# Kernel optimization log

Hardware: AMD Instinct MI355X
Metric: run time of the kernel (lower is better)

## Reference

```python
import jax, jax.numpy as jnp
import numpy as np

N = 128000   # total nodes (64 instances x 2000 nodes)
G = 64       # num graphs / instances
H = 128      # hidden_dim
IN = 3       # in_dim
L = 4        # embedding_l
E = 1024000
EPC = 512000
EMC = 512000
BN_EPS = 1e-5


def seg_mean(vals, idx, n):
    s = jax.ops.segment_sum(vals, idx, num_segments=n)
    c = jax.ops.segment_sum(jnp.ones((idx.shape[0], 1), vals.dtype), idx, num_segments=n)
    return s / jnp.maximum(c, 1.0)


def gin_layer(x, src, dst, W1, b1, g, beta, W2, b2):
    # GINConv(aggr='mean', eps=0): MLP(x + mean_{j->i} x_j), MLP = Lin-BN-ReLU-Lin
    agg = seg_mean(x[src], dst, N)
    z = (x + agg) @ W1 + b1
    mu = jnp.mean(z, axis=0)
    var = jnp.var(z, axis=0)
    z = (z - mu) / jnp.sqrt(var + BN_EPS) * g + beta   # BatchNorm1d (batch stats)
    z = jax.nn.relu(z)
    return z @ W2 + b2


def gat_conv(x, src, dst, W, asrc, adst, b):
    # PyG GATConv, heads=1: h=Wx; alpha=softmax_dst(leaky_relu(a_s.h_src + a_d.h_dst))
    h = x @ W                                           # [N, H]
    logits = jax.nn.leaky_relu((h * asrc).sum(-1)[src] + (h * adst).sum(-1)[dst], 0.2)
    m = jax.ops.segment_max(logits, dst, num_segments=N)
    a = jnp.exp(logits - m[dst])
    s = jax.ops.segment_sum(a, dst, num_segments=N)
    coef = a / (s[dst] + 1e-16)                         # self loops guarantee s > 0
    out = jax.ops.segment_sum(h[src] * coef[:, None], dst, num_segments=N)
    return out + b


def add_self_loops(ei):
    loops = jnp.arange(N, dtype=ei.dtype)
    return jnp.concatenate([ei[0], loops]), jnp.concatenate([ei[1], loops])


def setup_inputs() -> dict:
    key = jax.random.key(0)
    ks = iter(jax.random.split(key, 40))
    d = {}
    d['x'] = jax.random.normal(next(ks), (N, IN), dtype=jnp.float32)
    d['edge_index'] = jax.random.randint(next(ks), (2, E), 0, N)
    d['edge_index_pc'] = jax.random.randint(next(ks), (2, EPC), 0, N)
    d['edge_index_mc'] = jax.random.randint(next(ks), (2, EMC), 0, N)
    d['batch'] = jnp.repeat(jnp.arange(G), N // G)
    d['num_instances'] = G
    sc_in = 1.0 / np.sqrt(IN)
    sc_h = 1.0 / np.sqrt(H)
    # GIN layer 0 (in_dim=3) and layers 1..3 stacked
    d['gin0_W1'] = jax.random.normal(next(ks), (IN, H), jnp.float32) * sc_in
    d['gin0_b1'] = jnp.zeros((H,), jnp.float32)
    d['gin0_g'] = jnp.ones((H,), jnp.float32)
    d['gin0_beta'] = jnp.zeros((H,), jnp.float32)
    d['gin0_W2'] = jax.random.normal(next(ks), (H, H), jnp.float32) * sc_h
    d['gin0_b2'] = jnp.zeros((H,), jnp.float32)
    d['ginr_W1'] = jax.random.normal(next(ks), (L - 1, H, H), jnp.float32) * sc_h
    d['ginr_b1'] = jnp.zeros((L - 1, H), jnp.float32)
    d['ginr_g'] = jnp.ones((L - 1, H), jnp.float32)
    d['ginr_beta'] = jnp.zeros((L - 1, H), jnp.float32)
    d['ginr_W2'] = jax.random.normal(next(ks), (L - 1, H, H), jnp.float32) * sc_h
    d['ginr_b2'] = jnp.zeros((L - 1, H), jnp.float32)
    # DGHAN GAT params: layer 0 (in_dim=3), layers 1..3 (in=H); 2 convs (pc, mc) each
    d['gat0_W'] = jax.random.normal(next(ks), (2, IN, H), jnp.float32) * sc_in
    d['gat0_asrc'] = jax.random.normal(next(ks), (2, H), jnp.float32) * sc_h
    d['gat0_adst'] = jax.random.normal(next(ks), (2, H), jnp.float32) * sc_h
    d['gat0_bias'] = jnp.zeros((2, H), jnp.float32)
    d['gatr_W'] = jax.random.normal(next(ks), (L - 1, 2, H, H), jnp.float32) * sc_h
    d['gatr_asrc'] = jax.random.normal(next(ks), (L - 1, 2, H), jnp.float32) * sc_h
    d['gatr_adst'] = jax.random.normal(next(ks), (L - 1, 2, H), jnp.float32) * sc_h
    d['gatr_bias'] = jnp.zeros((L - 1, 2, H), jnp.float32)
    return d


def reference(x, edge_index, edge_index_pc, edge_index_mc, batch,
              gin0_W1, gin0_b1, gin0_g, gin0_beta, gin0_W2, gin0_b2,
              ginr_W1, ginr_b1, ginr_g, ginr_beta, ginr_W2, ginr_b2,
              gat0_W, gat0_asrc, gat0_adst, gat0_bias,
              gatr_W, gatr_asrc, gatr_adst, gatr_bias,
              num_instances):
    src, dst = edge_index[0], edge_index[1]
    # ---- GIN branch ----
    h = gin_layer(x, src, dst, gin0_W1, gin0_b1, gin0_g, gin0_beta, gin0_W2, gin0_b2)
    node_pool = h
    g_pool = seg_mean(h, batch, num_instances)
    for l in range(L - 1):
        h = gin_layer(h, src, dst, ginr_W1[l], ginr_b1[l], ginr_g[l], ginr_beta[l],
                      ginr_W2[l], ginr_b2[l])
        node_pool = node_pool + h
        g_pool = g_pool + seg_mean(h, batch, num_instances)
    # ---- DGHAN branch ----
    pc_src, pc_dst = add_self_loops(edge_index_pc)
    mc_src, mc_dst = add_self_loops(edge_index_mc)

    def dghan_layer(hn, W, asrc, adst, b):
        h_pc = jax.nn.elu(gat_conv(hn, pc_src, pc_dst, W[0], asrc[0], adst[0], b[0]))
        h_mc = jax.nn.elu(gat_conv(hn, mc_src, mc_dst, W[1], asrc[1], adst[1], b[1]))
        return 0.5 * (h_pc + h_mc)

    hd = dghan_layer(x, gat0_W, gat0_asrc, gat0_adst, gat0_bias)
    for l in range(L - 1):
        hd = dghan_layer(hd, gatr_W[l], gatr_asrc[l], gatr_adst[l], gatr_bias[l])
    graph_dghan = jnp.mean(hd.reshape(num_instances, -1, H), axis=1)
    # ---- fuse ----
    node_embed = jnp.concatenate([node_pool, hd], axis=-1)     # [N, 2H]
    graph_embed = jnp.concatenate([g_pool, graph_dghan], axis=-1)  # [G, 2H]
    return node_embed, graph_embed
```

## Files before the change

### kernel.cpp

```cpp
#include <hip/hip_runtime.h>
#include <cstdint>

#define NN 128000
#define GG 64
#define HH 128
#define EG 1024000
#define EPCV 512000
#define NPG 2000

static __device__ __forceinline__ float lrelu(float x){ return x > 0.f ? x : 0.2f*x; }
static __device__ __forceinline__ float f4get(const float4& v, int j){
  return j==0 ? v.x : j==1 ? v.y : j==2 ? v.z : v.w;
}

__global__ void k_seti(int* p, int n, int v){
  int i = blockIdx.x*blockDim.x + threadIdx.x;
  if(i < n) p[i] = v;
}
__global__ void k_setf(float* p, int n){
  int i = blockIdx.x*blockDim.x + threadIdx.x;
  if(i < n) p[i] = 0.f;
}

__global__ void k_hist(const int* __restrict__ dst, int E, int* __restrict__ counts){
  int i = blockIdx.x*blockDim.x + threadIdx.x;
  if(i < E) atomicAdd(&counts[dst[i]], 1);
}
__global__ void k_scan1(const int* __restrict__ counts, int* __restrict__ rowptr, int* __restrict__ bsums){
  __shared__ int lds[256];
  int t = threadIdx.x, b = blockIdx.x;
  int i0 = b*512 + t*2;
  int s0 = counts[i0], s1 = counts[i0+1];
  int pair = s0 + s1;
  lds[t] = pair; __syncthreads();
  for(int off=1; off<256; off<<=1){
    int v = (t >= off) ? lds[t-off] : 0;
    __syncthreads();
    lds[t] += v;
    __syncthreads();
  }
  int excl = lds[t] - pair;
  rowptr[i0+1] = excl + s0;
  rowptr[i0+2] = excl + pair;
  if(t == 255) bsums[b] = lds[t];
}
__global__ void k_scan2(int* bsums, int nb){
  __shared__ int lds[256];
  int t = threadIdx.x;
  int v = (t < nb) ? bsums[t] : 0;
  lds[t] = v; __syncthreads();
  for(int off=1; off<256; off<<=1){
    int u = (t >= off) ? lds[t-off] : 0;
    __syncthreads();
    lds[t] += u;
    __syncthreads();
  }
  if(t < nb) bsums[t] = lds[t] - v;
}
__global__ void k_scan3(int* __restrict__ rowptr, const int* __restrict__ bsums){
  int i = blockIdx.x*blockDim.x + threadIdx.x;
  if(i >= NN) return;
  rowptr[i+1] += bsums[i >> 9];
  if(i == 0) rowptr[0] = 0;
}
__global__ void k_fill(const int* __restrict__ rowptr, int* __restrict__ fill){
  int i = blockIdx.x*blockDim.x + threadIdx.x;
  if(i < NN) fill[i] = rowptr[i];
}
__global__ void k_scatter(const int* __restrict__ src, const int* __restrict__ dst, int E,
                          int* __restrict__ fill, int* __restrict__ colarr){
  int i = blockIdx.x*blockDim.x + threadIdx.x;
  if(i >= E) return;
  int pos = atomicAdd(&fill[dst[i]], 1);
  colarr[pos] = src[i];
}
__global__ void k_scatter_loops(int* __restrict__ fill, int* __restrict__ colarr){
  int i = blockIdx.x*blockDim.x + threadIdx.x;
  if(i >= NN) return;
  int pos = atomicAdd(&fill[i], 1);
  colarr[pos] = i;
}

__global__ __launch_bounds__(256) void k_segmean3(const float* __restrict__ x, const int* __restrict__ rp,
                           const int* __restrict__ col, float* __restrict__ y,
                           float* __restrict__ part){
  __shared__ float sp[4][9];
  int i = blockIdx.x*256 + threadIdx.x;
  int b = rp[i], e = rp[i+1];
  float a0=0.f, a1=0.f, a2=0.f;
  for(int j=b; j<e; ++j){
    int s = col[j];
    a0 += x[s*3]; a1 += x[s*3+1]; a2 += x[s*3+2];
  }
  float inv = 1.f / fmaxf((float)(e-b), 1.f);
  float y0 = x[i*3]   + a0*inv;
  float y1 = x[i*3+1] + a1*inv;
  float y2 = x[i*3+2] + a2*inv;
  y[i*3] = y0; y[i*3+1] = y1; y[i*3+2] = y2;
  float p[9] = {y0,y1,y2, y0*y0,y0*y1,y0*y2, y1*y1,y1*y2, y2*y2};
  #pragma unroll
  for(int off=1; off<64; off<<=1)
    #pragma unroll
    for(int j=0;j<9;++j) p[j] += __shfl_xor(p[j], off, 64);
  int lane = threadIdx.x & 63, wv = threadIdx.x >> 6;
  if(lane == 0)
    #pragma unroll
    for(int j=0;j<9;++j) sp[wv][j] = p[j];
  __syncthreads();
  int t = threadIdx.x;
  if(t < 9) part[blockIdx.x*9 + t] = sp[0][t] + sp[1][t] + sp[2][t] + sp[3][t];
}


__global__ __launch_bounds__(256) void k_segmean128(const float* __restrict__ h, const int* __restrict__ rp,
                             const int* __restrict__ col, float* __restrict__ y){
  int gid = blockIdx.x*256 + threadIdx.x;
  int w = gid >> 4, c0 = (gid & 15)*8;
  int b = rp[w], e = rp[w+1];
  float s0x=0.f,s0y=0.f,s0z=0.f,s0w=0.f, s1x=0.f,s1y=0.f,s1z=0.f,s1w=0.f;
  int j = b;
  for(; j+2 <= e; j += 2){
    int n0 = col[j], n1 = col[j+1];
    const float* p0 = h + (size_t)n0*HH + c0;
    const float* p1 = h + (size_t)n1*HH + c0;
    float4 u0 = *(const float4*)p0, u1 = *(const float4*)(p0+4);
    float4 v0 = *(const float4*)p1, v1 = *(const float4*)(p1+4);
    s0x += u0.x + v0.x; s0y += u0.y + v0.y; s0z += u0.z + v0.z; s0w += u0.w + v0.w;
    s1x += u1.x + v1.x; s1y += u1.y + v1.y; s1z += u1.z + v1.z; s1w += u1.w + v1.w;
  }
  if(j < e){
    const float* p0 = h + (size_t)col[j]*HH + c0;
    float4 u0 = *(const float4*)p0, u1 = *(const float4*)(p0+4);
    s0x += u0.x; s0y += u0.y; s0z += u0.z; s0w += u0.w;
    s1x += u1.x; s1y += u1.y; s1z += u1.z; s1w += u1.w;
  }
  float inv = 1.f / fmaxf((float)(e-b), 1.f);
  const float* sp = h + (size_t)w*HH + c0;
  float4 e0 = *(const float4*)sp, e1 = *(const float4*)(sp+4);
  float4 o0, o1;
  o0.x = e0.x + s0x*inv; o0.y = e0.y + s0y*inv; o0.z = e0.z + s0z*inv; o0.w = e0.w + s0w*inv;
  o1.x = e1.x + s1x*inv; o1.y = e1.y + s1y*inv; o1.z = e1.z + s1z*inv; o1.w = e1.w + s1w*inv;
  *(float4*)(y + (size_t)w*HH + c0)     = o0;
  *(float4*)(y + (size_t)w*HH + c0 + 4) = o1;
}

__global__ __launch_bounds__(256) void k_gat_agg(const float* __restrict__ hW, const int* __restrict__ rp,
                          const int* __restrict__ col, const float* __restrict__ sd,
                          const float* __restrict__ ddv, float* __restrict__ out,
                          const float* __restrict__ P, const float* __restrict__ bpc,
                          const float* __restrict__ bmc, float* __restrict__ out2){
  int gid = blockIdx.x*256 + threadIdx.x;
  int w = gid >> 4, c0 = (gid & 15)*8;
  int b = rp[w], e = rp[w+1];
  float dv = ddv[w];
  float s = 0.f;
  float a0x=0.f,a0y=0.f,a0z=0.f,a0w=0.f, a1x=0.f,a1y=0.f,a1z=0.f,a1w=0.f;
  int j = b;
  for(; j+2 <= e; j += 2){
    int n0 = col[j], n1 = col[j+1];
    float wt0 = expf(fminf(lrelu(sd[n0] + dv), 80.f));
    float wt1 = expf(fminf(lrelu(sd[n1] + dv), 80.f));
    const float* p0 = hW + (size_t)n0*HH + c0;
    const float* p1 = hW + (size_t)n1*HH + c0;
    float4 u0 = *(const float4*)p0, u1 = *(const float4*)(p0+4);
    float4 v0 = *(const float4*)p1, v1 = *(const float4*)(p1+4);
    s += wt0 + wt1;
    a0x += wt0*u0.x + wt1*v0.x; a0y += wt0*u0.y + wt1*v0.y;
    a0z += wt0*u0.z + wt1*v0.z; a0w += wt0*u0.w + wt1*v0.w;
    a1x += wt0*u1.x + wt1*v1.x; a1y += wt0*u1.y + wt1*v1.y;
    a1z += wt0*u1.z + wt1*v1.z; a1w += wt0*u1.w + wt1*v1.w;
  }
  if(j < e){
    int n0 = col[j];
    float wt0 = expf(fminf(lrelu(sd[n0] + dv), 80.f));
    const float* p0 = hW + (size_t)n0*HH + c0;
    float4 u0 = *(const float4*)p0, u1 = *(const float4*)(p0+4);
    s += wt0;
    a0x += wt0*u0.x; a0y += wt0*u0.y; a0z += wt0*u0.z; a0w += wt0*u0.w;
    a1x += wt0*u1.x; a1y += wt0*u1.y; a1z += wt0*u1.z; a1w += wt0*u1.w;
  }
  float inv = 1.f / (s + 1e-16f);
  a0x*=inv; a0y*=inv; a0z*=inv; a0w*=inv;
  a1x*=inv; a1y*=inv; a1z*=inv; a1w*=inv;
  if(P){
    const float* pp = P + (size_t)w*HH + c0;
    float4 p0 = *(const float4*)pp, p1 = *(const float4*)(pp+4);
    float4 bp0 = *(const float4*)(bpc + c0), bp1 = *(const float4*)(bpc + c0 + 4);
    float4 bm0 = *(const float4*)(bmc + c0), bm1 = *(const float4*)(bmc + c0 + 4);
    float q0 = p0.x + bp0.x; q0 = q0 > 0.f ? q0 : expm1f(q0);
    float q1 = p0.y + bp0.y; q1 = q1 > 0.f ? q1 : expm1f(q1);
    float q2 = p0.z + bp0.z; q2 = q2 > 0.f ? q2 : expm1f(q2);
    float q3 = p0.w + bp0.w; q3 = q3 > 0.f ? q3 : expm1f(q3);
    float q4 = p1.x + bp1.x; q4 = q4 > 0.f ? q4 : expm1f(q4);
    float q5 = p1.y + bp1.y; q5 = q5 > 0.f ? q5 : expm1f(q5);
    float q6 = p1.z + bp1.z; q6 = q6 > 0.f ? q6 : expm1f(q6);
    float q7 = p1.w + bp1.w; q7 = q7 > 0.f ? q7 : expm1f(q7);
    float r0 = a0x + bm0.x; r0 = r0 > 0.f ? r0 : expm1f(r0);
    float r1 = a0y + bm0.y; r1 = r1 > 0.f ? r1 : expm1f(r1);
    float r2 = a0z + bm0.z; r2 = r2 > 0.f ? r2 : expm1f(r2);
    float r3 = a0w + bm0.w; r3 = r3 > 0.f ? r3 : expm1f(r3);
    float r4 = a1x + bm1.x; r4 = r4 > 0.f ? r4 : expm1f(r4);
    float r5 = a1y + bm1.y; r5 = r5 > 0.f ? r5 : expm1f(r5);
    float r6 = a1z + bm1.z; r6 = r6 > 0.f ? r6 : expm1f(r6);
    float r7 = a1w + bm1.w; r7 = r7 > 0.f ? r7 : expm1f(r7);
    float4 o0 = make_float4(0.5f*(q0+r0), 0.5f*(q1+r1), 0.5f*(q2+r2), 0.5f*(q3+r3));
    float4 o1 = make_float4(0.5f*(q4+r4), 0.5f*(q5+r5), 0.5f*(q6+r6), 0.5f*(q7+r7));
    *(float4*)(out + (size_t)w*HH + c0)     = o0;
    *(float4*)(out + (size_t)w*HH + c0 + 4) = o1;
    if(out2){
      *(float4*)&out2[(size_t)w*256 + 128 + c0]     = o0;
      *(float4*)&out2[(size_t)w*256 + 128 + c0 + 4] = o1;
    }
  } else {
    *(float4*)(out + (size_t)w*HH + c0)     = make_float4(a0x, a0y, a0z, a0w);
    *(float4*)(out + (size_t)w*HH + c0 + 4) = make_float4(a1x, a1y, a1z, a1w);
  }
}

__global__ __launch_bounds__(256) void k_mm3(const float* __restrict__ A,
        const float* __restrict__ W,
        const float* __restrict__ asrc, const float* __restrict__ adst,
        float* __restrict__ sd, float* __restrict__ dd, float* __restrict__ out){
  int t = threadIdx.x;
  int r = blockIdx.x*8 + (t >> 5);
  int lane = t & 31, c0 = lane*4;
  float a0 = A[r*3], a1 = A[r*3+1], a2 = A[r*3+2];
  float v[4];
  #pragma unroll
  for(int j=0; j<4; ++j){
    int c = c0 + j;
    v[j] = a0*W[c] + a1*W[128+c] + a2*W[256+c];
  }
  *(float4*)&out[(size_t)r*128 + c0] = make_float4(v[0],v[1],v[2],v[3]);
  float s = 0.f, d = 0.f;
  #pragma unroll
  for(int j=0; j<4; ++j){ s += v[j]*asrc[c0+j]; d += v[j]*adst[c0+j]; }
  #pragma unroll
  for(int off=1; off<32; off<<=1){ s += __shfl_xor(s, off, 64); d += __shfl_xor(d, off, 64); }
  if(lane == 0){ sd[r] = s; dd[r] = d; }
}


#define MM_COMPUTE_CH(BUFIDX, K0) { \
  _Pragma("unroll") \
  for(int j_=0; j_<8; ++j_){ \
    float4 a0 = *(float4*)&sA[BUFIDX][j_][rg8]; \
    float4 a1 = *(float4*)&sA[BUFIDX][j_][rg8+4]; \
    float4 w0 = *(float4*)&sW[(K0)+j_][c0a]; \
    float4 w1 = *(float4*)&sW[(K0)+j_][c0b]; \
    float ar[8] = {a0.x,a0.y,a0.z,a0.w,a1.x,a1.y,a1.z,a1.w}; \
    _Pragma("unroll") \
    for(int rr_=0; rr_<8; ++rr_){ \
      acc[rr_][0] = fmaf(ar[rr_], w0.x, acc[rr_][0]); \
      acc[rr_][1] = fmaf(ar[rr_], w0.y, acc[rr_][1]); \
      acc[rr_][2] = fmaf(ar[rr_], w0.z, acc[rr_][2]); \
      acc[rr_][3] = fmaf(ar[rr_], w0.w, acc[rr_][3]); \
      acc[rr_][4] = fmaf(ar[rr_], w1.x, acc[rr_][4]); \
      acc[rr_][5] = fmaf(ar[rr_], w1.y, acc[rr_][5]); \
      acc[rr_][6] = fmaf(ar[rr_], w1.z, acc[rr_][6]); \
      acc[rr_][7] = fmaf(ar[rr_], w1.w, acc[rr_][7]); \
    } \
  } }

#define MM_STAGE(BUFIDX, CH, SRC) { \
  float4 sv_ = SRC; \
  if(HASBN){ \
    float4 ba_ = *(float4*)&sBNa[(CH)*8 + lk]; \
    float4 bs_ = *(float4*)&sBNsh[(CH)*8 + lk]; \
    sv_.x = fmaxf(fmaf(sv_.x, ba_.x, bs_.x), 0.f); \
    sv_.y = fmaxf(fmaf(sv_.y, ba_.y, bs_.y), 0.f); \
    sv_.z = fmaxf(fmaf(sv_.z, ba_.z, bs_.z), 0.f); \
    sv_.w = fmaxf(fmaf(sv_.w, ba_.w, bs_.w), 0.f); \
  } \
  sA[BUFIDX][lk  ][lrow] = sv_.x; \
  sA[BUFIDX][lk+1][lrow] = sv_.y; \
  sA[BUFIDX][lk+2][lrow] = sv_.z; \
  sA[BUFIDX][lk+3][lrow] = sv_.w; \
  }

template<bool HASBN>
__global__ __launch_bounds__(256) void k_mm128_t(
    const float* __restrict__ A,
    const float* __restrict__ bn_a, const float* __restrict__ bn_sh,
    const float* __restrict__ W, const float* __restrict__ bias,
    float* __restrict__ out, float* __restrict__ pool, int pool_mode,
    const float* __restrict__ asrc, const float* __restrict__ adst,
    float* __restrict__ sd, float* __restrict__ dd,
    float* __restrict__ musum, float* __restrict__ sqsum){
  __shared__ float sW[128][128];
  __shared__ float sA[2][8][128];
  __shared__ float sBNa[128], sBNsh[128];
  __shared__ float ls[128], lq[128];
  int t = threadIdx.x;
  #pragma unroll
  for(int i=0;i<16;++i){
    int f = i*1024 + t*4;
    *(float4*)&sW[f>>7][f&127] = *(const float4*)&W[f];
  }
  if(HASBN && t < 128){ sBNa[t] = bn_a[t]; sBNsh[t] = bn_sh[t]; }
  if(musum && t < 128){ ls[t] = 0.f; lq[t] = 0.f; }
  int row0 = blockIdx.x*128;
  int rg = t >> 4, cg = t & 15;
  int rg8 = rg*8;
  int c0a = cg*4, c0b = 64 + cg*4;
  int lrow = t >> 1, lk = (t & 1)*4;
  const float* ap = A + (size_t)(row0 + lrow)*HH + lk;
  float acc[8][8];
  #pragma unroll
  for(int i=0;i<8;++i)
    #pragma unroll
    for(int j=0;j<8;++j) acc[i][j]=0.f;
  float4 lv = *(const float4*)ap;
  __syncthreads();
  MM_STAGE(0, 0, lv);
  __syncthreads();

  #pragma unroll 1
  for(int ch=0; ch<16; ++ch){
    int b = ch & 1;
    float4 nlv = lv;
    if(ch < 15) nlv = *(const float4*)(ap + (ch+1)*8);
    MM_COMPUTE_CH(b, ch*8);
    if(ch < 15) MM_STAGE(b^1, ch+1, nlv);
    __syncthreads();
  }

  float as8[8], ad8[8];
  if(asrc){
    #pragma unroll
    for(int j=0;j<8;++j){
      int cj = (j<4) ? c0a+j : c0b+(j-4);
      as8[j] = asrc[cj]; ad8[j] = adst[cj];
    }
  }
  float bb[8];
  #pragma unroll
  for(int j=0;j<8;++j){
    int cj = (j<4) ? c0a+j : c0b+(j-4);
    bb[j] = bias ? bias[cj] : 0.f;
  }
  float cs[8], cq[8];
  #pragma unroll
  for(int j=0;j<8;++j){ cs[j]=0.f; cq[j]=0.f; }
  #pragma unroll
  for(int rr=0; rr<8; ++rr){
    int r = row0 + rg8 + rr;
    float v[8];
    #pragma unroll
    for(int j=0;j<8;++j) v[j] = acc[rr][j] + bb[j];
    *(float4*)&out[(size_t)r*128 + c0a] = make_float4(v[0],v[1],v[2],v[3]);
    *(float4*)&out[(size_t)r*128 + c0b] = make_float4(v[4],v[5],v[6],v[7]);
    if(pool_mode == 1){
      *(float4*)&pool[(size_t)r*256 + c0a] = make_float4(v[0],v[1],v[2],v[3]);
      *(float4*)&pool[(size_t)r*256 + c0b] = make_float4(v[4],v[5],v[6],v[7]);
    } else if(pool_mode == 2){
      float4 p0 = *(float4*)&pool[(size_t)r*256 + c0a];
      float4 p1 = *(float4*)&pool[(size_t)r*256 + c0b];
      p0.x+=v[0]; p0.y+=v[1]; p0.z+=v[2]; p0.w+=v[3];
      p1.x+=v[4]; p1.y+=v[5]; p1.z+=v[6]; p1.w+=v[7];
      *(float4*)&pool[(size_t)r*256 + c0a] = p0;
      *(float4*)&pool[(size_t)r*256 + c0b] = p1;
    }
    if(musum){
      #pragma unroll
      for(int j=0;j<8;++j){ cs[j] += v[j]; cq[j] += v[j]*v[j]; }
    }
    if(asrc){
      float s = 0.f, d = 0.f;
      #pragma unroll
      for(int j=0;j<8;++j){ s += v[j]*as8[j]; d += v[j]*ad8[j]; }
      #pragma unroll
      for(int off=1; off<16; off<<=1){ s += __shfl_xor(s, off, 64); d += __shfl_xor(d, off, 64); }
      if(cg == 0){ sd[r] = s; dd[r] = d; }
    }
  }
  if(musum){
    #pragma unroll
    for(int j=0;j<8;++j){
      int cj = (j<4) ? c0a+j : c0b+(j-4);
      atomicAdd(&ls[cj], cs[j]); atomicAdd(&lq[cj], cq[j]);
    }
    __syncthreads();
    if(t < 128){ atomicAdd(&musum[t], ls[t]); atomicAdd(&sqsum[t], lq[t]); }
  }
}

__global__ __launch_bounds__(256) void k_gin0(
    const float* __restrict__ y3,
    const float* __restrict__ W1, const float* __restrict__ b1,
    const float* __restrict__ bn_a, const float* __restrict__ bn_sh,
    const float* __restrict__ W2, const float* __restrict__ b2,
    float* __restrict__ outh, float* __restrict__ pool){
  __shared__ float sW[128][128];
  __shared__ float sW1[3][128];
  __shared__ float ssb[128];
  int t = threadIdx.x;
  #pragma unroll
  for(int i=0;i<16;++i){
    int f = i*1024 + t*4;
    *(float4*)&sW[f>>7][f&127] = *(const float4*)&W2[f];
  }
  if(t < 128){
    float a = bn_a[t];
    sW1[0][t] = W1[t]*a; sW1[1][t] = W1[128+t]*a; sW1[2][t] = W1[256+t]*a;
    ssb[t] = b1[t]*a + bn_sh[t];
  }
  int row0 = blockIdx.x*128;
  int rg = t >> 4, cg = t & 15;
  int c0a = cg*4, c0b = 64 + cg*4;
  float ya[8], yb[8], yc[8];
  #pragma unroll
  for(int rr=0; rr<8; ++rr){
    const float* yp = y3 + (size_t)(row0 + rg*8 + rr)*3;
    ya[rr] = yp[0]; yb[rr] = yp[1]; yc[rr] = yp[2];
  }
  float acc[8][8];
  #pragma unroll
  for(int i=0;i<8;++i)
    #pragma unroll
    for(int j=0;j<8;++j) acc[i][j]=0.f;
  __syncthreads();

  #pragma unroll 1
  for(int ch=0; ch<32; ++ch){
    int k0 = ch*4;
    float4 wa = *(float4*)&sW1[0][k0];
    float4 wb = *(float4*)&sW1[1][k0];
    float4 wc = *(float4*)&sW1[2][k0];
    float4 sb = *(float4*)&ssb[k0];
    float av[8][4];
    #pragma unroll
    for(int rr=0; rr<8; ++rr){
      #pragma unroll
      for(int j=0; j<4; ++j){
        av[rr][j] = fmaxf(fmaf(ya[rr], f4get(wa,j),
                         fmaf(yb[rr], f4get(wb,j),
                         fmaf(yc[rr], f4get(wc,j), f4get(sb,j)))), 0.f);
      }
    }
    #pragma unroll
    for(int j=0; j<4; ++j){
      float4 w0 = *(float4*)&sW[k0+j][c0a];
      float4 w1 = *(float4*)&sW[k0+j][c0b];
      #pragma unroll
      for(int rr=0; rr<8; ++rr){
        float a = av[rr][j];
        acc[rr][0] = fmaf(a, w0.x, acc[rr][0]);
        acc[rr][1] = fmaf(a, w0.y, acc[rr][1]);
        acc[rr][2] = fmaf(a, w0.z, acc[rr][2]);
        acc[rr][3] = fmaf(a, w0.w, acc[rr][3]);
        acc[rr][4] = fmaf(a, w1.x, acc[rr][4]);
        acc[rr][5] = fmaf(a, w1.y, acc[rr][5]);
        acc[rr][6] = fmaf(a, w1.z, acc[rr][6]);
        acc[rr][7] = fmaf(a, w1.w, acc[rr][7]);
      }
    }
  }
  #pragma unroll
  for(int rr=0; rr<8; ++rr){
    int r = row0 + rg*8 + rr;
    float v[8];
    #pragma unroll
    for(int j=0;j<8;++j){
      int cj = (j<4) ? c0a+j : c0b+(j-4);
      v[j] = acc[rr][j] + b2[cj];
    }
    float4 v0 = make_float4(v[0],v[1],v[2],v[3]);
    float4 v1 = make_float4(v[4],v[5],v[6],v[7]);
    *(float4*)&outh[(size_t)r*128 + c0a] = v0;
    *(float4*)&outh[(size_t)r*128 + c0b] = v1;
    *(float4*)&pool[(size_t)r*256 + c0a] = v0;
    *(float4*)&pool[(size_t)r*256 + c0b] = v1;
  }
}

__global__ void k_bnfin3(const float* __restrict__ part,
                         const float* __restrict__ W1, const float* __restrict__ b1,
                         const float* __restrict__ g, const float* __restrict__ beta,
                         float* __restrict__ a, float* __restrict__ sh){
  __shared__ float red[9][128];
  int t = threadIdx.x;
  float acc[9];
  #pragma unroll
  for(int j=0;j<9;++j) acc[j]=0.f;
  for(int i=t; i<500; i+=128)
    #pragma unroll
    for(int j=0;j<9;++j) acc[j] += part[i*9+j];
  #pragma unroll
  for(int j=0;j<9;++j) red[j][t] = acc[j];
  __syncthreads();
  for(int off=64; off; off>>=1){
    if(t < off)
      #pragma unroll
      for(int j=0;j<9;++j) red[j][t] += red[j][t+off];
    __syncthreads();
  }
  int c = t;
  double inv = 1.0/NN;
  double m0=red[0][0]*inv, m1=red[1][0]*inv, m2=red[2][0]*inv;
  double C00=red[3][0]*inv-m0*m0, C01=red[4][0]*inv-m0*m1, C02=red[5][0]*inv-m0*m2;
  double C11=red[6][0]*inv-m1*m1, C12=red[7][0]*inv-m1*m2, C22=red[8][0]*inv-m2*m2;
  double w0=W1[c], w1=W1[128+c], w2=W1[256+c];
  double mu  = m0*w0 + m1*w1 + m2*w2 + (double)b1[c];
  double var = w0*w0*C00 + w1*w1*C11 + w2*w2*C22
             + 2.0*(w0*w1*C01 + w0*w2*C02 + w1*w2*C12);
  double ai = (double)g[c] / sqrt(var + 1e-5);
  a[c]  = (float)ai;
  sh[c] = (float)((double)beta[c] - mu*ai);
}
__global__ void k_bnfin(const float* __restrict__ musum, const float* __restrict__ sqsum,
                        const float* __restrict__ g, const float* __restrict__ beta,
                        float* __restrict__ a, float* __restrict__ sh){
  int c = threadIdx.x;
  float mu  = musum[c] * (1.f/NN);
  float var = sqsum[c] * (1.f/NN) - mu*mu;
  float ai  = g[c] / sqrtf(var + 1e-5f);
  a[c]  = ai;
  sh[c] = beta[c] - mu*ai;
}

__global__ __launch_bounds__(256) void k_gpool2(const float* __restrict__ h,
                                                float* __restrict__ gpool, float scale){
  __shared__ float s[128];
  int g = blockIdx.x >> 4, chunk = blockIdx.x & 15;
  int t = threadIdx.x, c = t & 127, hh = t >> 7;
  int r0 = g*NPG + chunk*125;
  float sm = 0.f;
  for(int r = r0 + hh; r < r0 + 125; r += 2) sm += h[(size_t)r*128 + c];
  if(hh == 1) s[c] = sm;
  __syncthreads();
  if(hh == 0) atomicAdd(&gpool[g*128 + c], (sm + s[c]) * scale);
}
__global__ void k_write_graph(const float* __restrict__ gpool, const float* __restrict__ gdg,
                              float* __restrict__ out){
  int i = blockIdx.x*256 + threadIdx.x;
  int g = i >> 8, c = i & 255;
  out[(size_t)NN*256 + i] = (c < 128) ? gpool[g*128 + c] : gdg[g*128 + c - 128];
}

extern "C" void kernel_launch(void* const* d_in, const int* in_sizes, int n_in,
                              void* d_out, int out_size, void* d_ws, size_t ws_size,
                              hipStream_t stream){
  const float* x        = (const float*)d_in[0];
  const int*   ei       = (const int*)d_in[1];
  const int*   ei_pc    = (const int*)d_in[2];
  const int*   ei_mc    = (const int*)d_in[3];
  const float* gin0_W1  = (const float*)d_in[6];
  const float* gin0_b1  = (const float*)d_in[7];
  const float* gin0_g   = (const float*)d_in[8];
  const float* gin0_be  = (const float*)d_in[9];
  const float* gin0_W2  = (const float*)d_in[10];
  const float* gin0_b2  = (const float*)d_in[11];
  const float* ginr_W1  = (const float*)d_in[12];
  const float* ginr_b1  = (const float*)d_in[13];
  const float* ginr_g   = (const float*)d_in[14];
  const float* ginr_be  = (const float*)d_in[15];
  const float* ginr_W2  = (const float*)d_in[16];
  const float* ginr_b2  = (const float*)d_in[17];
  const float* gat0_W   = (const float*)d_in[18];
  const float* gat0_as  = (const float*)d_in[19];
  const float* gat0_ad  = (const float*)d_in[20];
  const float* gat0_b   = (const float*)d_in[21];
  const float* gatr_W   = (const float*)d_in[22];
  const float* gatr_as  = (const float*)d_in[23];
  const float* gatr_ad  = (const float*)d_in[24];
  const float* gatr_b   = (const float*)d_in[25];
  float* out = (float*)d_out;

  float* ws = (float*)d_ws;
  size_t o = 0;
  auto alloc_f = [&](size_t n){ float* p = ws + o; o += (n + 3) & ~(size_t)3; return p; };
  float* bufA   = alloc_f((size_t)NN*HH);
  float* bufB   = alloc_f((size_t)NN*HH);
  float* bufC   = alloc_f((size_t)NN*HH);
  int* rp_gin   = (int*)alloc_f(NN+1);
  int* col_gin  = (int*)alloc_f(EG);
  int* rp_pc    = (int*)alloc_f(NN+1);
  int* col_pc   = (int*)alloc_f(EPCV+NN);
  int* rp_mc    = (int*)alloc_f(NN+1);
  int* col_mc   = (int*)alloc_f(EPCV+NN);
  int* counts   = (int*)alloc_f(NN);
  int* bsums    = (int*)alloc_f(256);
  float* agg3   = alloc_f((size_t)NN*3);
  float* sd     = alloc_f(NN);
  float* dd     = alloc_f(NN);
  float* gpool  = alloc_f(GG*HH);
  float* gdg    = alloc_f(GG*HH);
  float* bnstat = alloc_f(256);
  float* bn_a   = alloc_f(128);
  float* bn_sh  = alloc_f(128);
  float* spart  = alloc_f(500*9 + 4);
  if(ws_size < o*sizeof(float)) return;

  dim3 B(256);
  dim3 gN((NN+255)/256);
  dim3 gQ(8000);
  dim3 gMM(1000), gMM3(16000);
  dim3 gGP(GG*16);

  auto build_csr = [&](const int* s, const int* d, int E, int loops, int* rp, int* colarr){
    k_seti<<<gN, B, 0, stream>>>(counts, NN, loops ? 1 : 0);
    k_hist<<<dim3((E+255)/256), B, 0, stream>>>(d, E, counts);
    k_scan1<<<dim3(250), B, 0, stream>>>(counts, rp, bsums);
    k_scan2<<<dim3(1), B, 0, stream>>>(bsums, 250);
    k_scan3<<<gN, B, 0, stream>>>(rp, bsums);
    k_fill<<<gN, B, 0, stream>>>(rp, counts);
    k_scatter<<<dim3((E+255)/256), B, 0, stream>>>(s, d, E, counts, colarr);
    if(loops) k_scatter_loops<<<gN, B, 0, stream>>>(counts, colarr);
  };
  build_csr(ei,           ei + EG,       EG,   0, rp_gin, col_gin);
  build_csr(ei_pc,        ei_pc + EPCV,  EPCV, 1, rp_pc,  col_pc);
  build_csr(ei_mc,        ei_mc + EPCV,  EPCV, 1, rp_mc,  col_mc);

  k_setf<<<dim3(64), B, 0, stream>>>(gpool, 2*GG*HH);

  k_segmean3<<<gN, B, 0, stream>>>(x, rp_gin, col_gin, agg3, spart);
  k_bnfin3<<<dim3(1), dim3(128), 0, stream>>>(spart, gin0_W1, gin0_b1, gin0_g, gin0_be, bn_a, bn_sh);
  k_gin0<<<gMM, B, 0, stream>>>(agg3, gin0_W1, gin0_b1, bn_a, bn_sh, gin0_W2, gin0_b2, bufA, out);
  k_gpool2<<<gGP, B, 0, stream>>>(bufA, gpool, 1.f/NPG);

  for(int l=0; l<3; ++l){
    k_segmean128<<<gQ, B, 0, stream>>>(bufA, rp_gin, col_gin, bufB);
    k_setf<<<dim3(1), B, 0, stream>>>(bnstat, 256);
    k_mm128_t<false><<<gMM, B, 0, stream>>>(bufB, nullptr, nullptr,
                                   ginr_W1 + (size_t)l*HH*HH, ginr_b1 + l*HH, bufC, nullptr, 0,
                                   nullptr, nullptr, nullptr, nullptr, bnstat, bnstat+128);
    k_bnfin<<<dim3(1), dim3(128), 0, stream>>>(bnstat, bnstat+128, ginr_g + l*HH, ginr_be + l*HH, bn_a, bn_sh);
    k_mm128_t<true><<<gMM, B, 0, stream>>>(bufC, bn_a, bn_sh,
                                   ginr_W2 + (size_t)l*HH*HH, ginr_b2 + l*HH, bufA, out, 2,
                                   nullptr, nullptr, nullptr, nullptr, nullptr, nullptr);
    k_gpool2<<<gGP, B, 0, stream>>>(bufA, gpool, 1.f/NPG);
  }

  k_mm3<<<gMM3, B, 0, stream>>>(x, gat0_W,          gat0_as,      gat0_ad,      sd, dd, bufB);
  k_gat_agg<<<gQ, B, 0, stream>>>(bufB, rp_pc, col_pc, sd, dd, bufC,
                                  nullptr, nullptr, nullptr, nullptr);
  k_mm3<<<gMM3, B, 0, stream>>>(x, gat0_W + 3*HH,   gat0_as + HH, gat0_ad + HH, sd, dd, bufB);
  k_gat_agg<<<gQ, B, 0, stream>>>(bufB, rp_mc, col_mc, sd, dd, bufA,
                                  bufC, gat0_b, gat0_b + HH, nullptr);

  for(int l=0; l<3; ++l){
    const float* Wl = gatr_W + (size_t)l*2*HH*HH;
    k_mm128_t<false><<<gMM, B, 0, stream>>>(bufA, nullptr, nullptr, Wl, nullptr, bufB, nullptr, 0,
                                   gatr_as + (size_t)(l*2)*HH, gatr_ad + (size_t)(l*2)*HH, sd, dd,
                                   nullptr, nullptr);
    k_gat_agg<<<gQ, B, 0, stream>>>(bufB, rp_pc, col_pc, sd, dd, bufC,
                                    nullptr, nullptr, nullptr, nullptr);
    k_mm128_t<false><<<gMM, B, 0, stream>>>(bufA, nullptr, nullptr, Wl + HH*HH, nullptr, bufB, nullptr, 0,
                                   gatr_as + (size_t)(l*2+1)*HH, gatr_ad + (size_t)(l*2+1)*HH, sd, dd,
                                   nullptr, nullptr);
    k_gat_agg<<<gQ, B, 0, stream>>>(bufB, rp_mc, col_mc, sd, dd, bufA,
                                    bufC, gatr_b + (size_t)(l*2)*HH, gatr_b + (size_t)(l*2+1)*HH,
                                    (l == 2) ? out : nullptr);
  }

  k_gpool2<<<gGP, B, 0, stream>>>(bufA, gdg, 1.f/NPG);
  k_write_graph<<<dim3(GG), B, 0, stream>>>(gpool, gdg, out);
}
```

Before: 2.309 ms.

## Replace FP32 SIMT 128x128 GEMMs with split-bf16 MFMA kernels

Replaces the shared-memory FP32 FMA GEMM with an MFMA kernel that splits each FP32 operand into high and low bf16 halves. It computes three bf16 MFMA products (lo*hi, hi*lo, hi*hi) to keep close to FP32 accuracy. Weights are pre-split and transposed once per call by a new k_wsplit kernel. Activations are loaded straight from global into registers, with no LDS staging. The epilogue now writes scalar per-column stores instead of float4 and reduces BN stats and attention dots with shuffles, which may hurt store coalescing.

```diff
diff --git a/kernel.cpp b/kernel.cpp
--- a/kernel.cpp
+++ b/kernel.cpp
@@ -8,9 +8,23 @@
 #define EPCV 512000
 #define NPG 2000
 
+typedef unsigned short u16;
+typedef __attribute__((ext_vector_type(8))) short bf16x8;
+typedef __attribute__((ext_vector_type(4))) float f32x4;
+
 static __device__ __forceinline__ float lrelu(float x){ return x > 0.f ? x : 0.2f*x; }
 static __device__ __forceinline__ float f4get(const float4& v, int j){
   return j==0 ? v.x : j==1 ? v.y : j==2 ? v.z : v.w;
+}
+static __device__ __forceinline__ void splitf(const float* v8, bf16x8& hi, bf16x8& lo){
+  #pragma unroll
+  for(int i=0;i<8;++i){
+    uint32_t u = __float_as_uint(v8[i]);
+    float hf = __uint_as_float(u & 0xFFFF0000u);
+    float lf = v8[i] - hf;
+    hi[i] = (short)(u >> 16);
+    lo[i] = (short)(__float_as_uint(lf) >> 16);
+  }
 }
 
 __global__ void k_seti(int* p, int n, int v){
@@ -240,145 +254,151 @@
   if(lane == 0){ sd[r] = s; dd[r] = d; }
 }
 
-
-#define MM_COMPUTE_CH(BUFIDX, K0) { \
-  _Pragma("unroll") \
-  for(int j_=0; j_<8; ++j_){ \
-    float4 a0 = *(float4*)&sA[BUFIDX][j_][rg8]; \
-    float4 a1 = *(float4*)&sA[BUFIDX][j_][rg8+4]; \
-    float4 w0 = *(float4*)&sW[(K0)+j_][c0a]; \
-    float4 w1 = *(float4*)&sW[(K0)+j_][c0b]; \
-    float ar[8] = {a0.x,a0.y,a0.z,a0.w,a1.x,a1.y,a1.z,a1.w}; \
-    _Pragma("unroll") \
-    for(int rr_=0; rr_<8; ++rr_){ \
-      acc[rr_][0] = fmaf(ar[rr_], w0.x, acc[rr_][0]); \
-      acc[rr_][1] = fmaf(ar[rr_], w0.y, acc[rr_][1]); \
-      acc[rr_][2] = fmaf(ar[rr_], w0.z, acc[rr_][2]); \
-      acc[rr_][3] = fmaf(ar[rr_], w0.w, acc[rr_][3]); \
-      acc[rr_][4] = fmaf(ar[rr_], w1.x, acc[rr_][4]); \
-      acc[rr_][5] = fmaf(ar[rr_], w1.y, acc[rr_][5]); \
-      acc[rr_][6] = fmaf(ar[rr_], w1.z, acc[rr_][6]); \
-      acc[rr_][7] = fmaf(ar[rr_], w1.w, acc[rr_][7]); \
-    } \
-  } }
-
-#define MM_STAGE(BUFIDX, CH, SRC) { \
-  float4 sv_ = SRC; \
-  if(HASBN){ \
-    float4 ba_ = *(float4*)&sBNa[(CH)*8 + lk]; \
-    float4 bs_ = *(float4*)&sBNsh[(CH)*8 + lk]; \
-    sv_.x = fmaxf(fmaf(sv_.x, ba_.x, bs_.x), 0.f); \
-    sv_.y = fmaxf(fmaf(sv_.y, ba_.y, bs_.y), 0.f); \
-    sv_.z = fmaxf(fmaf(sv_.z, ba_.z, bs_.z), 0.f); \
-    sv_.w = fmaxf(fmaf(sv_.w, ba_.w, bs_.w), 0.f); \
-  } \
-  sA[BUFIDX][lk  ][lrow] = sv_.x; \
-  sA[BUFIDX][lk+1][lrow] = sv_.y; \
-  sA[BUFIDX][lk+2][lrow] = sv_.z; \
-  sA[BUFIDX][lk+3][lrow] = sv_.w; \
-  }
+__global__ __launch_bounds__(256) void k_wsplit(const float* __restrict__ W,
+                                                u16* __restrict__ wh, u16* __restrict__ wl){
+  int m = blockIdx.x >> 6, part = blockIdx.x & 63;
+  int idx = part*256 + threadIdx.x;
+  int k = idx >> 7, c = idx & 127;
+  float a = W[(size_t)m*16384 + idx];
+  uint32_t u = __float_as_uint(a);
+  float lf = a - __uint_as_float(u & 0xFFFF0000u);
+  size_t o = (size_t)m*16384 + (size_t)c*128 + k;
+  wh[o] = (u16)(u >> 16);
+  wl[o] = (u16)(__float_as_uint(lf) >> 16);
+}
 
 template<bool HASBN>
-__global__ __launch_bounds__(256) void k_mm128_t(
+__global__ __launch_bounds__(256) void k_mmfma(
     const float* __restrict__ A,
     const float* __restrict__ bn_a, const float* __restrict__ bn_sh,
-    const float* __restrict__ W, const float* __restrict__ bias,
+    const u16* __restrict__ WhT, const u16* __restrict__ WlT,
+    const float* __restrict__ bias,
     float* __restrict__ out, float* __restrict__ pool, int pool_mode,
     const float* __restrict__ asrc, const float* __restrict__ adst,
     float* __restrict__ sd, float* __restrict__ dd,
     float* __restrict__ musum, float* __restrict__ sqsum){
-  __shared__ float sW[128][128];
-  __shared__ float sA[2][8][128];
-  __shared__ float sBNa[128], sBNsh[128];
   __shared__ float ls[128], lq[128];
   int t = threadIdx.x;
-  #pragma unroll
-  for(int i=0;i<16;++i){
-    int f = i*1024 + t*4;
-    *(float4*)&sW[f>>7][f&127] = *(const float4*)&W[f];
-  }
-  if(HASBN && t < 128){ sBNa[t] = bn_a[t]; sBNsh[t] = bn_sh[t]; }
-  if(musum && t < 128){ ls[t] = 0.f; lq[t] = 0.f; }
-  int row0 = blockIdx.x*128;
-  int rg = t >> 4, cg = t & 15;
-  int rg8 = rg*8;
-  int c0a = cg*4, c0b = 64 + cg*4;
-  int lrow = t >> 1, lk = (t & 1)*4;
-  const float* ap = A + (size_t)(row0 + lrow)*HH + lk;
-  float acc[8][8];
-  #pragma unroll
-  for(int i=0;i<8;++i)
-    #pragma unroll
-    for(int j=0;j<8;++j) acc[i][j]=0.f;
-  float4 lv = *(const float4*)ap;
-  __syncthreads();
-  MM_STAGE(0, 0, lv);
-  __syncthreads();
-
-  #pragma unroll 1
-  for(int ch=0; ch<16; ++ch){
-    int b = ch & 1;
-    float4 nlv = lv;
-    if(ch < 15) nlv = *(const float4*)(ap + (ch+1)*8);
-    MM_COMPUTE_CH(b, ch*8);
-    if(ch < 15) MM_STAGE(b^1, ch+1, nlv);
+  if(musum){
+    if(t < 128){ ls[t] = 0.f; lq[t] = 0.f; }
     __syncthreads();
+  }
+  int w = t >> 6, l = t & 63;
+  int lrow = l & 15, lkg = l >> 4;
+  int rowbase = blockIdx.x*128 + w*32;
+
+  bf16x8 ah[2][4], al[2][4];
+  #pragma unroll
+  for(int rt=0; rt<2; ++rt){
+    int r = rowbase + rt*16 + lrow;
+    #pragma unroll
+    for(int ks=0; ks<4; ++ks){
+      int k0 = ks*32 + lkg*8;
+      const float* ap = A + (size_t)r*HH + k0;
+      float av[8];
+      *(float4*)&av[0] = *(const float4*)ap;
+      *(float4*)&av[4] = *(const float4*)(ap+4);
+      if(HASBN){
+        float4 ba0 = *(const float4*)(bn_a + k0), ba1 = *(const float4*)(bn_a + k0 + 4);
+        float4 bs0 = *(const float4*)(bn_sh + k0), bs1 = *(const float4*)(bn_sh + k0 + 4);
+        av[0] = fmaxf(fmaf(av[0], ba0.x, bs0.x), 0.f);
+        av[1] = fmaxf(fmaf(av[1], ba0.y, bs0.y), 0.f);
+        av[2] = fmaxf(fmaf(av[2], ba0.z, bs0.z), 0.f);
+        av[3] = fmaxf(fmaf(av[3], ba0.w, bs0.w), 0.f);
+        av[4] = fmaxf(fmaf(av[4], ba1.x, bs1.x), 0.f);
+        av[5] = fmaxf(fmaf(av[5], ba1.y, bs1.y), 0.f);
+        av[6] = fmaxf(fmaf(av[6], ba1.z, bs1.z), 0.f);
+        av[7] = fmaxf(fmaf(av[7], ba1.w, bs1.w), 0.f);
+      }
+      splitf(av, ah[rt][ks], al[rt][ks]);
+    }
+  }
+
+  f32x4 acc[2][8];
+  bf16x8 bh[4], bl[4], nbh[4], nbl[4];
+  #pragma unroll
+  for(int ks=0; ks<4; ++ks){
+    int k0 = ks*32 + lkg*8;
+    bh[ks] = *(const bf16x8*)(WhT + (size_t)lrow*HH + k0);
+    bl[ks] = *(const bf16x8*)(WlT + (size_t)lrow*HH + k0);
+  }
+  #pragma unroll
+  for(int ct=0; ct<8; ++ct){
+    if(ct < 7){
+      int col = (ct+1)*16 + lrow;
+      #pragma unroll
+      for(int ks=0; ks<4; ++ks){
+        int k0 = ks*32 + lkg*8;
+        nbh[ks] = *(const bf16x8*)(WhT + (size_t)col*HH + k0);
+        nbl[ks] = *(const bf16x8*)(WlT + (size_t)col*HH + k0);
+      }
+    }
+    #pragma unroll
+    for(int rt=0; rt<2; ++rt){
+      f32x4 a = {0.f, 0.f, 0.f, 0.f};
+      #pragma unroll
+      for(int ks=0; ks<4; ++ks){
+        a = __builtin_amdgcn_mfma_f32_16x16x32_bf16(al[rt][ks], bh[ks], a, 0, 0, 0);
+        a = __builtin_amdgcn_mfma_f32_16x16x32_bf16(ah[rt][ks], bl[ks], a, 0, 0, 0);
+        a = __builtin_amdgcn_mfma_f32_16x16x32_bf16(ah[rt][ks], bh[ks], a, 0, 0, 0);
+      }
+      acc[rt][ct] = a;
+    }
+    if(ct < 7){
+      #pragma unroll
+      for(int ks=0; ks<4; ++ks){ bh[ks] = nbh[ks]; bl[ks] = nbl[ks]; }
+    }
   }
 
   float as8[8], ad8[8];
   if(asrc){
     #pragma unroll
-    for(int j=0;j<8;++j){
-      int cj = (j<4) ? c0a+j : c0b+(j-4);
-      as8[j] = asrc[cj]; ad8[j] = adst[cj];
-    }
+    for(int ct=0; ct<8; ++ct){ as8[ct] = asrc[ct*16+lrow]; ad8[ct] = adst[ct*16+lrow]; }
   }
   float bb[8];
   #pragma unroll
-  for(int j=0;j<8;++j){
-    int cj = (j<4) ? c0a+j : c0b+(j-4);
-    bb[j] = bias ? bias[cj] : 0.f;
-  }
+  for(int ct=0; ct<8; ++ct) bb[ct] = bias ? bias[ct*16+lrow] : 0.f;
   float cs[8], cq[8];
   #pragma unroll
-  for(int j=0;j<8;++j){ cs[j]=0.f; cq[j]=0.f; }
-  #pragma unroll
-  for(int rr=0; rr<8; ++rr){
-    int r = row0 + rg8 + rr;
-    float v[8];
-    #pragma unroll
-    for(int j=0;j<8;++j) v[j] = acc[rr][j] + bb[j];
-    *(float4*)&out[(size_t)r*128 + c0a] = make_float4(v[0],v[1],v[2],v[3]);
-    *(float4*)&out[(size_t)r*128 + c0b] = make_float4(v[4],v[5],v[6],v[7]);
-    if(pool_mode == 1){
-      *(float4*)&pool[(size_t)r*256 + c0a] = make_float4(v[0],v[1],v[2],v[3]);
-      *(float4*)&pool[(size_t)r*256 + c0b] = make_float4(v[4],v[5],v[6],v[7]);
-    } else if(pool_mode == 2){
-      float4 p0 = *(float4*)&pool[(size_t)r*256 + c0a];
-      float4 p1 = *(float4*)&pool[(size_t)r*256 + c0b];
-      p0.x+=v[0]; p0.y+=v[1]; p0.z+=v[2]; p0.w+=v[3];
-      p1.x+=v[4]; p1.y+=v[5]; p1.z+=v[6]; p1.w+=v[7];
-      *(float4*)&pool[(size_t)r*256 + c0a] = p0;
-      *(float4*)&pool[(size_t)r*256 + c0b] = p1;
-    }
-    if(musum){
-      #pragma unroll
-      for(int j=0;j<8;++j){ cs[j] += v[j]; cq[j] += v[j]*v[j]; }
-    }
-    if(asrc){
-      float s = 0.f, d = 0.f;
-      #pragma unroll
-      for(int j=0;j<8;++j){ s += v[j]*as8[j]; d += v[j]*ad8[j]; }
-      #pragma unroll
-      for(int off=1; off<16; off<<=1){ s += __shfl_xor(s, off, 64); d += __shfl_xor(d, off, 64); }
-      if(cg == 0){ sd[r] = s; dd[r] = d; }
+  for(int ct=0; ct<8; ++ct){ cs[ct]=0.f; cq[ct]=0.f; }
+  #pragma unroll
+  for(int rt=0; rt<2; ++rt){
+    #pragma unroll
+    for(int j=0; j<4; ++j){
+      int r = rowbase + rt*16 + lkg*4 + j;
+      float sdot = 0.f, ddot = 0.f;
+      #pragma unroll
+      for(int ct=0; ct<8; ++ct){
+        float v = acc[rt][ct][j] + bb[ct];
+        int c = ct*16 + lrow;
+        out[(size_t)r*HH + c] = v;
+        if(pool_mode == 1) pool[(size_t)r*256 + c] = v;
+        else if(pool_mode == 2) pool[(size_t)r*256 + c] += v;
+        if(musum){ cs[ct] += v; cq[ct] += v*v; }
+        if(asrc){ sdot += v*as8[ct]; ddot += v*ad8[ct]; }
+      }
+      if(asrc){
+        #pragma unroll
+        for(int off=1; off<16; off<<=1){
+          sdot += __shfl_xor(sdot, off, 64);
+          ddot += __shfl_xor(ddot, off, 64);
+        }
+        if(lrow == 0){ sd[r] = sdot; dd[r] = ddot; }
+      }
     }
   }
   if(musum){
     #pragma unroll
-    for(int j=0;j<8;++j){
-      int cj = (j<4) ? c0a+j : c0b+(j-4);
-      atomicAdd(&ls[cj], cs[j]); atomicAdd(&lq[cj], cq[j]);
+    for(int ct=0; ct<8; ++ct){
+      #pragma unroll
+      for(int off=16; off<64; off<<=1){
+        cs[ct] += __shfl_xor(cs[ct], off, 64);
+        cq[ct] += __shfl_xor(cq[ct], off, 64);
+      }
+      if(lkg == 0){
+        atomicAdd(&ls[ct*16+lrow], cs[ct]);
+        atomicAdd(&lq[ct*16+lrow], cq[ct]);
+      }
     }
     __syncthreads();
     if(t < 128){ atomicAdd(&musum[t], ls[t]); atomicAdd(&sqsum[t], lq[t]); }
@@ -590,6 +610,10 @@
   float* bn_a   = alloc_f(128);
   float* bn_sh  = alloc_f(128);
   float* spart  = alloc_f(500*9 + 4);
+  float* whbuf  = alloc_f(12*16384/2);
+  float* wlbuf  = alloc_f(12*16384/2);
+  u16* wh = (u16*)whbuf;
+  u16* wl = (u16*)wlbuf;
   if(ws_size < o*sizeof(float)) return;
 
   dim3 B(256);
@@ -614,6 +638,10 @@
 
   k_setf<<<dim3(64), B, 0, stream>>>(gpool, 2*GG*HH);
 
+  k_wsplit<<<dim3(3*64), B, 0, stream>>>(ginr_W1, wh,           wl);
+  k_wsplit<<<dim3(3*64), B, 0, stream>>>(ginr_W2, wh + 3*16384, wl + 3*16384);
+  k_wsplit<<<dim3(6*64), B, 0, stream>>>(gatr_W,  wh + 6*16384, wl + 6*16384);
+
   k_segmean3<<<gN, B, 0, stream>>>(x, rp_gin, col_gin, agg3, spart);
   k_bnfin3<<<dim3(1), dim3(128), 0, stream>>>(spart, gin0_W1, gin0_b1, gin0_g, gin0_be, bn_a, bn_sh);
   k_gin0<<<gMM, B, 0, stream>>>(agg3, gin0_W1, gin0_b1, bn_a, bn_sh, gin0_W2, gin0_b2, bufA, out);
@@ -622,12 +650,14 @@
   for(int l=0; l<3; ++l){
     k_segmean128<<<gQ, B, 0, stream>>>(bufA, rp_gin, col_gin, bufB);
     k_setf<<<dim3(1), B, 0, stream>>>(bnstat, 256);
-    k_mm128_t<false><<<gMM, B, 0, stream>>>(bufB, nullptr, nullptr,
-                                   ginr_W1 + (size_t)l*HH*HH, ginr_b1 + l*HH, bufC, nullptr, 0,
+    k_mmfma<false><<<gMM, B, 0, stream>>>(bufB, nullptr, nullptr,
+                                   wh + (size_t)l*16384, wl + (size_t)l*16384,
+                                   ginr_b1 + l*HH, bufC, nullptr, 0,
                                    nullptr, nullptr, nullptr, nullptr, bnstat, bnstat+128);
     k_bnfin<<<dim3(1), dim3(128), 0, stream>>>(bnstat, bnstat+128, ginr_g + l*HH, ginr_be + l*HH, bn_a, bn_sh);
-    k_mm128_t<true><<<gMM, B, 0, stream>>>(bufC, bn_a, bn_sh,
-                                   ginr_W2 + (size_t)l*HH*HH, ginr_b2 + l*HH, bufA, out, 2,
+    k_mmfma<true><<<gMM, B, 0, stream>>>(bufC, bn_a, bn_sh,
+                                   wh + (size_t)(3+l)*16384, wl + (size_t)(3+l)*16384,
+                                   ginr_b2 + l*HH, bufA, out, 2,
                                    nullptr, nullptr, nullptr, nullptr, nullptr, nullptr);
     k_gpool2<<<gGP, B, 0, stream>>>(bufA, gpool, 1.f/NPG);
   }
@@ -640,13 +670,16 @@
                                   bufC, gat0_b, gat0_b + HH, nullptr);
 
   for(int l=0; l<3; ++l){
-    const float* Wl = gatr_W + (size_t)l*2*HH*HH;
-    k_mm128_t<false><<<gMM, B, 0, stream>>>(bufA, nullptr, nullptr, Wl, nullptr, bufB, nullptr, 0,
+    k_mmfma<false><<<gMM, B, 0, stream>>>(bufA, nullptr, nullptr,
+                                   wh + (size_t)(6+l*2)*16384, wl + (size_t)(6+l*2)*16384,
+                                   nullptr, bufB, nullptr, 0,
                                    gatr_as + (size_t)(l*2)*HH, gatr_ad + (size_t)(l*2)*HH, sd, dd,
                                    nullptr, nullptr);
     k_gat_agg<<<gQ, B, 0, stream>>>(bufB, rp_pc, col_pc, sd, dd, bufC,
                                     nullptr, nullptr, nullptr, nullptr);
-    k_mm128_t<false><<<gMM, B, 0, stream>>>(bufA, nullptr, nullptr, Wl + HH*HH, nullptr, bufB, nullptr, 0,
+    k_mmfma<false><<<gMM, B, 0, stream>>>(bufA, nullptr, nullptr,
+                                   wh + (size_t)(7+l*2)*16384, wl + (size_t)(7+l*2)*16384,
+                                   nullptr, bufB, nullptr, 0,
                                    gatr_as + (size_t)(l*2+1)*HH, gatr_ad + (size_t)(l*2+1)*HH, sd, dd,
                                    nullptr, nullptr);
     k_gat_agg<<<gQ, B, 0, stream>>>(bufB, rp_mc, col_mc, sd, dd, bufA,
```

New measurement: 2.347 ms. About the same (+1.6%).
